# Optimization experiments

Hardware: AMD Instinct MI355X
Metric: run time of the kernel (lower is better)

The kernel has to match this reference:

```python
import jax, jax.numpy as jnp
import numpy as np

# IO parameters (aihwkit-style preset)
INP_BOUND = 1.0
INP_RES = 1.0 / 254.0      # 8-bit DAC: 2^8 - 2 levels
OUT_BOUND = 12.0
OUT_RES = 1.0 / 510.0      # 9-bit ADC: 2^9 - 2 levels
OUT_NOISE = 0.06
OUT_SCALE = 1.0
MAX_BM_FACTOR = 1000.0
MAX_BM_RES = 0.25
INP_RES_EFF = 2.0 * INP_BOUND * INP_RES  # effective input grid step (bm escape test)


def _quantize_st(x, res, bound):
    # UniformQuantize: round to grid of step (res * 2 * bound), straight-through grad
    r = (1.0 / res if res > 1.0 else res) * 2.0 * bound
    q = jnp.round(x / r) * r
    return x + jax.lax.stop_gradient(q - x)


def _one_pass(input_, weight, nm, reduction, rnd, key):
    """One analog MVM pass at a given bound-management reduction factor."""
    scale = 1.0 / (nm * reduction)                      # [m, 1]
    x = input_ * scale                                  # noise/bound managed input
    x = _quantize_st(x, INP_RES, INP_BOUND)             # DAC discretization
    x = jnp.clip(x, -INP_BOUND, INP_BOUND)              # DAC clipping
    out = x @ weight.T                                  # [m, out_size] analog GEMM
    noise = OUT_NOISE * jax.random.normal(
        jax.random.fold_in(key, rnd), out.shape, out.dtype)
    out = out + noise                                   # output (ADC) noise
    out = _quantize_st(out, OUT_RES, OUT_BOUND)         # ADC discretization
    not_clipping = jnp.all((out <= OUT_BOUND) & (out >= -OUT_BOUND))
    out = jnp.clip(out, -OUT_BOUND, OUT_BOUND)          # ADC saturation
    return not_clipping, out


def setup_inputs() -> dict:
    key = jax.random.key(0)
    k1, k2 = jax.random.split(key)
    input_ = jax.random.normal(k1, (8192, 4096), jnp.float32)
    # 0.1 std weights -> outputs mostly within ADC bound after 1-2 bm rounds
    weight = 0.1 * jax.random.normal(k2, (4096, 4096), jnp.float32)
    return {"input_": input_, "weight": weight}


def reference(input_, weight):
    key = jax.random.key(42)
    # noise management: ABS_MAX over the input dimension (nm_thres <= 0 -> no clamp)
    nm = jnp.max(jnp.abs(input_), axis=-1, keepdims=True)
    nm = jnp.where(nm <= 0.0, 1.0, nm)
    out_shape = input_.shape[:-1] + (weight.shape[0],)

    def cond(c):
        return ~c[2]

    def body(c):
        rnd, red, _, _ = c
        red = red * 2.0          # reduction_due_to_bound_management *= 2
        rnd = rnd + 1
        passed, out = _one_pass(input_, weight, nm, red, rnd, key)
        passed = passed | (red > MAX_BM_FACTOR) | (red > MAX_BM_RES / INP_RES_EFF)
        return (rnd, red, passed, out)

    init = (jnp.int32(0), jnp.float32(0.5), jnp.array(False),
            jnp.zeros(out_shape, input_.dtype))
    _, red, _, out = jax.lax.while_loop(cond, body, init)
    # undo the input scaling: output *= out_scale / scale = out_scale * nm * red
    return out * (OUT_SCALE * nm * red)
```

## Files before the change

### kernel.cpp

```cpp
#include <hip/hip_runtime.h>
#include <stdint.h>


#define MM 8192
#define KK 4096
#define NN 4096
#define TOTAL_OUT ((size_t)MM * (size_t)NN)
#define GEMM_BLOCKS 2048
#define NT (KK / 64)

typedef __attribute__((ext_vector_type(4))) float f32x4;
typedef __attribute__((ext_vector_type(8))) short bf16x8;
typedef __attribute__((ext_vector_type(8))) unsigned short u16x8;

#define R_IN_F ((float)(2.0 / 254.0))
#define R_OUT_F ((float)(24.0 / 510.0))

struct BmState {
  int done;
  float red_final;
  int viol[8];
  int ctr[8];
};

__host__ __device__ __forceinline__ uint32_t tf_rotl(uint32_t v, int r) {
  return (v << r) | (v >> (32 - r));
}

__host__ __device__ __forceinline__ void threefry2x32(uint32_t k0, uint32_t k1,
                                                      uint32_t x0, uint32_t x1,
                                                      uint32_t &o0, uint32_t &o1) {
  uint32_t ks2 = k0 ^ k1 ^ 0x1BD11BDAu;
  x0 += k0; x1 += k1;
#define TF_R(r) { x0 += x1; x1 = tf_rotl(x1, r); x1 ^= x0; }
  TF_R(13) TF_R(15) TF_R(26) TF_R(6)
  x0 += k1; x1 += ks2 + 1u;
  TF_R(17) TF_R(29) TF_R(16) TF_R(24)
  x0 += ks2; x1 += k0 + 2u;
  TF_R(13) TF_R(15) TF_R(26) TF_R(6)
  x0 += k0; x1 += k1 + 3u;
  TF_R(17) TF_R(29) TF_R(16) TF_R(24)
  x0 += k1; x1 += ks2 + 4u;
  TF_R(13) TF_R(15) TF_R(26) TF_R(6)
  x0 += ks2; x1 += k0 + 5u;
#undef TF_R
  o0 = x0; o1 = x1;
}

__device__ __forceinline__ float erfinv_xla(float x) {
  float w = -log1pf(-x * x);
  float p;
  if (w < 5.0f) {
    w = w - 2.5f;
    p = 2.81022636e-08f;
    p = fmaf(p, w, 3.43273939e-07f);
    p = fmaf(p, w, -3.5233877e-06f);
    p = fmaf(p, w, -4.39150654e-06f);
    p = fmaf(p, w, 0.00021858087f);
    p = fmaf(p, w, -0.00125372503f);
    p = fmaf(p, w, -0.00417768164f);
    p = fmaf(p, w, 0.246640727f);
    p = fmaf(p, w, 1.50140941f);
  } else {
    w = sqrtf(w) - 3.0f;
    p = -0.000200214257f;
    p = fmaf(p, w, 0.000100950558f);
    p = fmaf(p, w, 0.00134934322f);
    p = fmaf(p, w, -0.00367342844f);
    p = fmaf(p, w, 0.00573950773f);
    p = fmaf(p, w, -0.0076224613f);
    p = fmaf(p, w, 0.00943887047f);
    p = fmaf(p, w, 1.00167406f);
    p = fmaf(p, w, 2.83297682f);
  }
  return p * x;
}

__device__ __forceinline__ float noise_from_bits(uint32_t bits) {
  uint32_t fb = (bits >> 9) | 0x3f800000u;
  float f = __uint_as_float(fb) - 1.0f;
  const float lo = -0.99999994f;
  float u = f * 2.0f + lo;
  u = fmaxf(lo, u);
  return 0.06f * (1.41421356f * erfinv_xla(u));
}

__device__ __forceinline__ unsigned short bf16_rne(float f) {
  uint32_t x = __float_as_uint(f);
  x += 0x7fffu + ((x >> 16) & 1u);
  return (unsigned short)(x >> 16);
}

__device__ __forceinline__ float dac_quant(float v, float s) {
  float x = v * s;
  float t = x / R_IN_F;
  float k = rintf(t);
  return fminf(127.0f, fmaxf(-127.0f, k));
}

__device__ __forceinline__ u16x8 quant8(float4 a, float4 b, float s) {
  u16x8 o;
  o[0] = bf16_rne(dac_quant(a.x, s));
  o[1] = bf16_rne(dac_quant(a.y, s));
  o[2] = bf16_rne(dac_quant(a.z, s));
  o[3] = bf16_rne(dac_quant(a.w, s));
  o[4] = bf16_rne(dac_quant(b.x, s));
  o[5] = bf16_rne(dac_quant(b.y, s));
  o[6] = bf16_rne(dac_quant(b.z, s));
  o[7] = bf16_rne(dac_quant(b.w, s));
  return o;
}

__device__ __forceinline__ u16x8 conv8(float4 a, float4 b) {
  u16x8 o;
  o[0] = bf16_rne(a.x); o[1] = bf16_rne(a.y); o[2] = bf16_rne(a.z); o[3] = bf16_rne(a.w);
  o[4] = bf16_rne(b.x); o[5] = bf16_rne(b.y); o[6] = bf16_rne(b.z); o[7] = bf16_rne(b.w);
  return o;
}

__device__ __forceinline__ float adc_one(float gval, size_t idx, float sc,
                                         uint32_t fk0, uint32_t fk1, bool &bad) {
  uint32_t w0, w1;
  threefry2x32(fk0, fk1, 0u, (uint32_t)idx, w0, w1);
  float o = R_IN_F * gval + noise_from_bits(w0 ^ w1);
  float q = rintf(o / R_OUT_F) * R_OUT_F;
  float z = o + (q - o);
  bad = bad || (z > 12.0f) || (z < -12.0f);
  z = fminf(12.0f, fmaxf(-12.0f, z));
  return z * sc;
}

__device__ __forceinline__ void fin_tail(BmState *st, int pass, float red, int nblocks,
                                         bool bad) {
  unsigned long long vb = __ballot(bad ? 1 : 0);
  if (vb != 0ull && (threadIdx.x & 63) == 0) atomicOr(&st->viol[pass], 1);
  __syncthreads();
  if (threadIdx.x == 0) {
    __threadfence();
    int prev = atomicAdd(&st->ctr[pass], 1);
    if (prev == nblocks - 1) {
      int viol = atomicOr(&st->viol[pass], 0);
      bool ok = (viol == 0) || (red > 1000.0f) || (red > 31.75f);
      if (ok) {
        st->done = 1;
        st->red_final = red;
      }
    }
  }
}

__global__ __launch_bounds__(256) void k_rowquant(const float *__restrict__ in,
                                                  float *__restrict__ nm,
                                                  unsigned short *__restrict__ ab,
                                                  BmState *st) {
  if (blockIdx.x == 0 && threadIdx.x == 0) {
    st->done = 0;
    st->red_final = 0.0f;
    for (int i = 0; i < 8; ++i) { st->viol[i] = 0; st->ctr[i] = 0; }
  }
  const int row = blockIdx.x;
  const float *r = in + (size_t)row * KK;
  const int t = threadIdx.x;
  float4 a0 = *(const float4 *)(r + t * 8);
  float4 a1 = *(const float4 *)(r + t * 8 + 4);
  float4 b0 = *(const float4 *)(r + 2048 + t * 8);
  float4 b1 = *(const float4 *)(r + 2048 + t * 8 + 4);
  float m = 0.0f;
  m = fmaxf(m, fmaxf(fmaxf(fabsf(a0.x), fabsf(a0.y)), fmaxf(fabsf(a0.z), fabsf(a0.w))));
  m = fmaxf(m, fmaxf(fmaxf(fabsf(a1.x), fabsf(a1.y)), fmaxf(fabsf(a1.z), fabsf(a1.w))));
  m = fmaxf(m, fmaxf(fmaxf(fabsf(b0.x), fabsf(b0.y)), fmaxf(fabsf(b0.z), fabsf(b0.w))));
  m = fmaxf(m, fmaxf(fmaxf(fabsf(b1.x), fabsf(b1.y)), fmaxf(fabsf(b1.z), fabsf(b1.w))));
#pragma unroll
  for (int off = 32; off > 0; off >>= 1) m = fmaxf(m, __shfl_down(m, off));
  __shared__ float wm[4];
  if ((t & 63) == 0) wm[t >> 6] = m;
  __syncthreads();
  const float mm = fmaxf(fmaxf(wm[0], wm[1]), fmaxf(wm[2], wm[3]));
  const float nmv = (mm <= 0.0f) ? 1.0f : mm;
  if (t == 0) nm[row] = nmv;
  const float s = 1.0f / (nmv * 1.0f);
  unsigned short *o = ab + (size_t)row * KK;
  *(u16x8 *)(o + t * 8) = quant8(a0, a1, s);
  *(u16x8 *)(o + 2048 + t * 8) = quant8(b0, b1, s);
}

__global__ __launch_bounds__(256) void k_rowmax(const float *__restrict__ in,
                                                float *__restrict__ nm, BmState *st) {
  if (blockIdx.x == 0 && threadIdx.x == 0) {
    st->done = 0;
    st->red_final = 0.0f;
    for (int i = 0; i < 8; ++i) { st->viol[i] = 0; st->ctr[i] = 0; }
  }
  const int row = blockIdx.x;
  const float4 *r = (const float4 *)(in + (size_t)row * KK);
  const int t = threadIdx.x;
  float m = 0.0f;
#pragma unroll
  for (int i = 0; i < 4; ++i) {
    float4 v = r[t + i * 256];
    m = fmaxf(m, fmaxf(fmaxf(fabsf(v.x), fabsf(v.y)), fmaxf(fabsf(v.z), fabsf(v.w))));
  }
#pragma unroll
  for (int off = 32; off > 0; off >>= 1) m = fmaxf(m, __shfl_down(m, off));
  __shared__ float wm[4];
  if ((t & 63) == 0) wm[t >> 6] = m;
  __syncthreads();
  if (t == 0) {
    m = fmaxf(fmaxf(wm[0], wm[1]), fmaxf(wm[2], wm[3]));
    nm[row] = (m <= 0.0f) ? 1.0f : m;
  }
}

__global__ __launch_bounds__(256) void k_wconv(const float *__restrict__ w,
                                               unsigned short *__restrict__ wb) {
  const size_t idx = ((size_t)blockIdx.x * 256 + threadIdx.x) * 8;
  float4 a = *(const float4 *)(w + idx);
  float4 b = *(const float4 *)(w + idx + 4);
  *(u16x8 *)(wb + idx) = conv8(a, b);
}

__device__ __forceinline__ void async16(const void *g, void *l) {
  __builtin_amdgcn_global_load_lds((const __attribute__((address_space(1))) uint32_t *)g,
                                   (__attribute__((address_space(3))) uint32_t *)l,
                                   16, 0, 0);
}

__global__ __launch_bounds__(512, 1) void k_gemm(const unsigned short *__restrict__ A,
                                                 const unsigned short *__restrict__ B,
                                                 float *__restrict__ C) {
  __shared__ unsigned short As[2][256 * 64];
  __shared__ unsigned short Bs[2][256 * 64];
  const int tid = threadIdx.x;
  const int lane = tid & 63;
  const int wv = tid >> 6;
  const int wr = wv >> 2;
  const int wc = wv & 3;
  const int brow = blockIdx.y * 256;
  const int bcol = blockIdx.x * 256;

  f32x4 acc[8][4];
#pragma unroll
  for (int m = 0; m < 8; ++m)
#pragma unroll
    for (int n = 0; n < 4; ++n) acc[m][n] = (f32x4){0.f, 0.f, 0.f, 0.f};

  int sr[4], sk8[4];
#pragma unroll
  for (int i = 0; i < 4; ++i) {
    const int u = i * 512 + tid;
    sr[i] = u >> 3;
    sk8[i] = ((u & 7) ^ (sr[i] & 7)) * 8;
  }

#define STAGE(buf, kt)                                                                 \
  {                                                                                    \
    _Pragma("unroll") for (int i = 0; i < 4; ++i) {                                    \
      const int ub = i * 512 + wv * 64;                \
      async16(A + (size_t)(brow + sr[i]) * KK + (kt) * 64 + sk8[i],                    \
              (char *)As[buf] + (size_t)ub * 16);                                      \
      async16(B + (size_t)(bcol + sr[i]) * KK + (kt) * 64 + sk8[i],                    \
              (char *)Bs[buf] + (size_t)ub * 16);                                      \
    }                                                                                  \
  }

  STAGE(0, 0);

  const int r16 = lane & 15;
  const int kg = (lane >> 4) * 8;

#pragma unroll 2
  for (int kt = 0; kt < NT; ++kt) {
    const int cur = kt & 1;
    if (kt + 1 < NT) {
      STAGE(cur ^ 1, kt + 1);
      asm volatile("s_waitcnt vmcnt(8)" ::: "memory");
    } else {
      asm volatile("s_waitcnt vmcnt(0)" ::: "memory");
    }
    __builtin_amdgcn_s_barrier();

#pragma unroll
    for (int kk = 0; kk < 64; kk += 32) {
      const int ck = (kk + kg) >> 3;
      bf16x8 af[8], bg[4];
#pragma unroll
      for (int m = 0; m < 8; ++m) {
        const int ra = wr * 128 + m * 16 + r16;
        af[m] = *(const bf16x8 *)(As[cur] + ra * 64 + ((ck ^ (ra & 7)) << 3));
      }
#pragma unroll
      for (int n = 0; n < 4; ++n) {
        const int rb = wc * 64 + n * 16 + r16;
        bg[n] = *(const bf16x8 *)(Bs[cur] + rb * 64 + ((ck ^ (rb & 7)) << 3));
      }
#pragma unroll
      for (int m = 0; m < 8; ++m)
#pragma unroll
        for (int n = 0; n < 4; ++n)
          acc[m][n] = __builtin_amdgcn_mfma_f32_16x16x32_bf16(af[m], bg[n], acc[m][n], 0, 0, 0);
    }
    __builtin_amdgcn_sched_barrier(0);
    __builtin_amdgcn_s_barrier();
  }
#undef STAGE

  const int c16 = lane & 15;
  const int q4 = (lane >> 4) * 4;
#pragma unroll
  for (int m = 0; m < 8; ++m) {
    const int row = brow + wr * 128 + m * 16 + q4;
#pragma unroll
    for (int n = 0; n < 4; ++n) {
      const int col = bcol + wc * 64 + n * 16 + c16;
      float *cp = C + (size_t)row * NN + col;
      cp[0 * (size_t)NN] = acc[m][n][0];
      cp[1 * (size_t)NN] = acc[m][n][1];
      cp[2 * (size_t)NN] = acc[m][n][2];
      cp[3 * (size_t)NN] = acc[m][n][3];
    }
  }
}

__global__ __launch_bounds__(256) void k_epi(float *__restrict__ out,
                                             const float *__restrict__ nm,
                                             BmState *__restrict__ st, int pass, float red,
                                             uint32_t fk0, uint32_t fk1) {
  const size_t idx = ((size_t)blockIdx.x * 256 + threadIdx.x) * 8;
  const int row = (int)(idx >> 12);
  const float sc = nm[row] * red;
  float4 a = *(const float4 *)(out + idx);
  float4 b = *(const float4 *)(out + idx + 4);
  float v[8] = {a.x, a.y, a.z, a.w, b.x, b.y, b.z, b.w};
  bool bad = false;
#pragma unroll
  for (int j = 0; j < 8; ++j) v[j] = adc_one(v[j], idx + j, sc, fk0, fk1, bad);
  *(float4 *)(out + idx) = make_float4(v[0], v[1], v[2], v[3]);
  *(float4 *)(out + idx + 4) = make_float4(v[4], v[5], v[6], v[7]);
  unsigned long long vb = __ballot(bad ? 1 : 0);
  if (vb != 0ull && (threadIdx.x & 63) == 0) atomicOr(&st->viol[pass], 1);
}

__global__ void k_fin(BmState *st, int pass, float red) {
  if (st->done) return;
  bool ok = (st->viol[pass] == 0) || (red > 1000.0f) || (red > 31.75f);
  if (ok) {
    st->done = 1;
    st->red_final = red;
  }
}

__global__ __launch_bounds__(256) void k_retry(const float *__restrict__ Af,
                                               const float *__restrict__ Bf,
                                               const float *__restrict__ nm, float red,
                                               float *__restrict__ C,
                                               BmState *__restrict__ st, int pass,
                                               uint32_t fk0, uint32_t fk1) {
  if (st->done) return;
  __shared__ unsigned short As[128 * 64];
  __shared__ unsigned short Bs[128 * 64];
  const int tid = threadIdx.x;
  const int lane = tid & 63;
  const int wv = tid >> 6;
  const int wr = wv >> 1, wc = wv & 1;
  const int brow = blockIdx.y * 128;
  const int bcol = blockIdx.x * 128;

  f32x4 acc[4][4];
#pragma unroll
  for (int m = 0; m < 4; ++m)
#pragma unroll
    for (int n = 0; n < 4; ++n) acc[m][n] = (f32x4){0.f, 0.f, 0.f, 0.f};

  float sA[4];
#pragma unroll
  for (int i = 0; i < 4; ++i) {
    int u = i * 256 + tid;
    sA[i] = 1.0f / (nm[brow + (u >> 3)] * red);
  }

  for (int kt = 0; kt < KK; kt += 64) {
#pragma unroll
    for (int i = 0; i < 4; ++i) {
      const int u = i * 256 + tid;
      const int r = u >> 3, k8 = (u & 7) * 8;
      {
        const float *g = Af + (size_t)(brow + r) * KK + kt + k8;
        float4 x = *(const float4 *)g, y = *(const float4 *)(g + 4);
        *(u16x8 *)(As + r * 64 + k8) = quant8(x, y, sA[i]);
      }
      {
        const float *g = Bf + (size_t)(bcol + r) * KK + kt + k8;
        float4 x = *(const float4 *)g, y = *(const float4 *)(g + 4);
        *(u16x8 *)(Bs + r * 64 + k8) = conv8(x, y);
      }
    }
    __syncthreads();

    const int r16 = lane & 15;
    const int kg = (lane >> 4) * 8;
#pragma unroll
    for (int kk = 0; kk < 64; kk += 32) {
      bf16x8 af[4], bg[4];
#pragma unroll
      for (int m = 0; m < 4; ++m)
        af[m] = *(const bf16x8 *)(As + (wr * 64 + m * 16 + r16) * 64 + kk + kg);
#pragma unroll
      for (int n = 0; n < 4; ++n)
        bg[n] = *(const bf16x8 *)(Bs + (wc * 64 + n * 16 + r16) * 64 + kk + kg);
#pragma unroll
      for (int m = 0; m < 4; ++m)
#pragma unroll
        for (int n = 0; n < 4; ++n)
          acc[m][n] = __builtin_amdgcn_mfma_f32_16x16x32_bf16(af[m], bg[n], acc[m][n], 0, 0, 0);
    }
    __syncthreads();
  }

  const int c16 = lane & 15;
  const int q4 = (lane >> 4) * 4;
  bool bad = false;
#pragma unroll
  for (int m = 0; m < 4; ++m) {
    const int row0 = brow + wr * 64 + m * 16 + q4;
#pragma unroll
    for (int j = 0; j < 4; ++j) {
      const int row = row0 + j;
      const float sc = nm[row] * red;
#pragma unroll
      for (int n = 0; n < 4; ++n) {
        const int col = bcol + wc * 64 + n * 16 + c16;
        const size_t idx = (size_t)row * NN + col;
        C[idx] = adc_one(acc[m][n][j], idx, sc, fk0, fk1, bad);
      }
    }
  }
  fin_tail(st, pass, red, GEMM_BLOCKS, bad);
}

extern "C" void kernel_launch(void *const *d_in, const int *in_sizes, int n_in,
                              void *d_out, int out_size, void *d_ws, size_t ws_size,
                              hipStream_t stream) {
  const float *input = (const float *)d_in[0];
  const float *weight = (const float *)d_in[1];
  if (n_in >= 2 && in_sizes[0] < in_sizes[1]) {
    const float *t = input; input = weight; weight = t;
  }
  float *out = (float *)d_out;
  char *ws = (char *)d_ws;
  BmState *st = (BmState *)ws;
  float *nm = (float *)(ws + 4096);
  unsigned short *Ab = (unsigned short *)(ws + 36864);
  unsigned short *Wb = Ab + (size_t)MM * KK;
  const size_t need = 36864 + ((size_t)MM * KK + (size_t)NN * KK) * 2;
  const bool fast = ws_size >= need;

  uint32_t fk[8][2];
  for (int p = 1; p <= 6; ++p) threefry2x32(0u, 42u, 0u, (uint32_t)p, fk[p][0], fk[p][1]);

  if (fast) {
    k_rowquant<<<dim3(MM), dim3(256), 0, stream>>>(input, nm, Ab, st);
    k_wconv<<<dim3((NN * (size_t)KK) / 2048), dim3(256), 0, stream>>>(weight, Wb);
    k_gemm<<<dim3(NN / 256, MM / 256), dim3(512), 0, stream>>>(Ab, Wb, out);
    k_epi<<<dim3((int)(TOTAL_OUT / 2048)), dim3(256), 0, stream>>>(out, nm, st, 1, 1.0f,
                                                                   fk[1][0], fk[1][1]);
    k_fin<<<dim3(1), dim3(1), 0, stream>>>(st, 1, 1.0f);
  } else {
    k_rowmax<<<dim3(MM), dim3(256), 0, stream>>>(input, nm, st);
    k_retry<<<dim3(NN / 128, MM / 128), dim3(256), 0, stream>>>(
        input, weight, nm, 1.0f, out, st, 1, fk[1][0], fk[1][1]);
  }

  float red = 2.0f;
  for (int p = 2; p <= 6; ++p, red *= 2.0f) {
    k_retry<<<dim3(NN / 128, MM / 128), dim3(256), 0, stream>>>(
        input, weight, nm, red, out, st, p, fk[p][0], fk[p][1]);
  }
}
```

Before: 495.9 us.

## Fuse ADC epilogue into GEMM and merge input/weight prep kernels

The separate ADC epilogue kernel (noise, quantize, clip, violation detection) now runs inside the GEMM's register epilogue, so the 128 MB fp32 output is no longer written, re-read and rewritten. The row-quantize and weight-convert kernels are merged into one launch to save a launch and let the two workloads overlap. In exchange the GEMM epilogue carries the per-element RNG work, which raises register pressure and lengthens the tail of the GEMM.

```diff
diff --git a/kernel.cpp b/kernel.cpp
--- a/kernel.cpp
+++ b/kernel.cpp
@@ -149,39 +149,48 @@
   }
 }
 
-__global__ __launch_bounds__(256) void k_rowquant(const float *__restrict__ in,
-                                                  float *__restrict__ nm,
-                                                  unsigned short *__restrict__ ab,
-                                                  BmState *st) {
-  if (blockIdx.x == 0 && threadIdx.x == 0) {
-    st->done = 0;
-    st->red_final = 0.0f;
-    for (int i = 0; i < 8; ++i) { st->viol[i] = 0; st->ctr[i] = 0; }
-  }
-  const int row = blockIdx.x;
-  const float *r = in + (size_t)row * KK;
+__global__ __launch_bounds__(256) void k_prep(const float *__restrict__ in,
+                                              const float *__restrict__ w,
+                                              float *__restrict__ nm,
+                                              unsigned short *__restrict__ ab,
+                                              unsigned short *__restrict__ wb,
+                                              BmState *st) {
   const int t = threadIdx.x;
-  float4 a0 = *(const float4 *)(r + t * 8);
-  float4 a1 = *(const float4 *)(r + t * 8 + 4);
-  float4 b0 = *(const float4 *)(r + 2048 + t * 8);
-  float4 b1 = *(const float4 *)(r + 2048 + t * 8 + 4);
-  float m = 0.0f;
-  m = fmaxf(m, fmaxf(fmaxf(fabsf(a0.x), fabsf(a0.y)), fmaxf(fabsf(a0.z), fabsf(a0.w))));
-  m = fmaxf(m, fmaxf(fmaxf(fabsf(a1.x), fabsf(a1.y)), fmaxf(fabsf(a1.z), fabsf(a1.w))));
-  m = fmaxf(m, fmaxf(fmaxf(fabsf(b0.x), fabsf(b0.y)), fmaxf(fabsf(b0.z), fabsf(b0.w))));
-  m = fmaxf(m, fmaxf(fmaxf(fabsf(b1.x), fabsf(b1.y)), fmaxf(fabsf(b1.z), fabsf(b1.w))));
-#pragma unroll
-  for (int off = 32; off > 0; off >>= 1) m = fmaxf(m, __shfl_down(m, off));
-  __shared__ float wm[4];
-  if ((t & 63) == 0) wm[t >> 6] = m;
-  __syncthreads();
-  const float mm = fmaxf(fmaxf(wm[0], wm[1]), fmaxf(wm[2], wm[3]));
-  const float nmv = (mm <= 0.0f) ? 1.0f : mm;
-  if (t == 0) nm[row] = nmv;
-  const float s = 1.0f / (nmv * 1.0f);
-  unsigned short *o = ab + (size_t)row * KK;
-  *(u16x8 *)(o + t * 8) = quant8(a0, a1, s);
-  *(u16x8 *)(o + 2048 + t * 8) = quant8(b0, b1, s);
+  if (blockIdx.x < MM) {
+    if (blockIdx.x == 0 && t == 0) {
+      st->done = 0;
+      st->red_final = 0.0f;
+      for (int i = 0; i < 8; ++i) { st->viol[i] = 0; st->ctr[i] = 0; }
+    }
+    const int row = blockIdx.x;
+    const float *r = in + (size_t)row * KK;
+    float4 a0 = *(const float4 *)(r + t * 8);
+    float4 a1 = *(const float4 *)(r + t * 8 + 4);
+    float4 b0 = *(const float4 *)(r + 2048 + t * 8);
+    float4 b1 = *(const float4 *)(r + 2048 + t * 8 + 4);
+    float m = 0.0f;
+    m = fmaxf(m, fmaxf(fmaxf(fabsf(a0.x), fabsf(a0.y)), fmaxf(fabsf(a0.z), fabsf(a0.w))));
+    m = fmaxf(m, fmaxf(fmaxf(fabsf(a1.x), fabsf(a1.y)), fmaxf(fabsf(a1.z), fabsf(a1.w))));
+    m = fmaxf(m, fmaxf(fmaxf(fabsf(b0.x), fabsf(b0.y)), fmaxf(fabsf(b0.z), fabsf(b0.w))));
+    m = fmaxf(m, fmaxf(fmaxf(fabsf(b1.x), fabsf(b1.y)), fmaxf(fabsf(b1.z), fabsf(b1.w))));
+#pragma unroll
+    for (int off = 32; off > 0; off >>= 1) m = fmaxf(m, __shfl_down(m, off));
+    __shared__ float wm[4];
+    if ((t & 63) == 0) wm[t >> 6] = m;
+    __syncthreads();
+    const float mm = fmaxf(fmaxf(wm[0], wm[1]), fmaxf(wm[2], wm[3]));
+    const float nmv = (mm <= 0.0f) ? 1.0f : mm;
+    if (t == 0) nm[row] = nmv;
+    const float s = 1.0f / (nmv * 1.0f);
+    unsigned short *o = ab + (size_t)row * KK;
+    *(u16x8 *)(o + t * 8) = quant8(a0, a1, s);
+    *(u16x8 *)(o + 2048 + t * 8) = quant8(b0, b1, s);
+  } else {
+    const size_t idx = ((size_t)(blockIdx.x - MM) * 256 + t) * 8;
+    float4 a = *(const float4 *)(w + idx);
+    float4 b = *(const float4 *)(w + idx + 4);
+    *(u16x8 *)(wb + idx) = conv8(a, b);
+  }
 }
 
 __global__ __launch_bounds__(256) void k_rowmax(const float *__restrict__ in,
@@ -211,14 +220,6 @@
   }
 }
 
-__global__ __launch_bounds__(256) void k_wconv(const float *__restrict__ w,
-                                               unsigned short *__restrict__ wb) {
-  const size_t idx = ((size_t)blockIdx.x * 256 + threadIdx.x) * 8;
-  float4 a = *(const float4 *)(w + idx);
-  float4 b = *(const float4 *)(w + idx + 4);
-  *(u16x8 *)(wb + idx) = conv8(a, b);
-}
-
 __device__ __forceinline__ void async16(const void *g, void *l) {
   __builtin_amdgcn_global_load_lds((const __attribute__((address_space(1))) uint32_t *)g,
                                    (__attribute__((address_space(3))) uint32_t *)l,
@@ -227,7 +228,10 @@
 
 __global__ __launch_bounds__(512, 1) void k_gemm(const unsigned short *__restrict__ A,
                                                  const unsigned short *__restrict__ B,
-                                                 float *__restrict__ C) {
+                                                 const float *__restrict__ nm,
+                                                 float *__restrict__ C,
+                                                 BmState *__restrict__ st, int pass,
+                                                 float red, uint32_t fk0, uint32_t fk1) {
   __shared__ unsigned short As[2][256 * 64];
   __shared__ unsigned short Bs[2][256 * 64];
   const int tid = threadIdx.x;
@@ -306,38 +310,24 @@
 
   const int c16 = lane & 15;
   const int q4 = (lane >> 4) * 4;
+  bool bad = false;
 #pragma unroll
   for (int m = 0; m < 8; ++m) {
-    const int row = brow + wr * 128 + m * 16 + q4;
-#pragma unroll
-    for (int n = 0; n < 4; ++n) {
-      const int col = bcol + wc * 64 + n * 16 + c16;
-      float *cp = C + (size_t)row * NN + col;
-      cp[0 * (size_t)NN] = acc[m][n][0];
-      cp[1 * (size_t)NN] = acc[m][n][1];
-      cp[2 * (size_t)NN] = acc[m][n][2];
-      cp[3 * (size_t)NN] = acc[m][n][3];
-    }
-  }
-}
-
-__global__ __launch_bounds__(256) void k_epi(float *__restrict__ out,
-                                             const float *__restrict__ nm,
-                                             BmState *__restrict__ st, int pass, float red,
-                                             uint32_t fk0, uint32_t fk1) {
-  const size_t idx = ((size_t)blockIdx.x * 256 + threadIdx.x) * 8;
-  const int row = (int)(idx >> 12);
-  const float sc = nm[row] * red;
-  float4 a = *(const float4 *)(out + idx);
-  float4 b = *(const float4 *)(out + idx + 4);
-  float v[8] = {a.x, a.y, a.z, a.w, b.x, b.y, b.z, b.w};
-  bool bad = false;
-#pragma unroll
-  for (int j = 0; j < 8; ++j) v[j] = adc_one(v[j], idx + j, sc, fk0, fk1, bad);
-  *(float4 *)(out + idx) = make_float4(v[0], v[1], v[2], v[3]);
-  *(float4 *)(out + idx + 4) = make_float4(v[4], v[5], v[6], v[7]);
+    const int row0 = brow + wr * 128 + m * 16 + q4;
+#pragma unroll
+    for (int j = 0; j < 4; ++j) {
+      const int row = row0 + j;
+      const float sc = nm[row] * red;
+#pragma unroll
+      for (int n = 0; n < 4; ++n) {
+        const int col = bcol + wc * 64 + n * 16 + c16;
+        const size_t idx = (size_t)row * NN + col;
+        C[idx] = adc_one(acc[m][n][j], idx, sc, fk0, fk1, bad);
+      }
+    }
+  }
   unsigned long long vb = __ballot(bad ? 1 : 0);
-  if (vb != 0ull && (threadIdx.x & 63) == 0) atomicOr(&st->viol[pass], 1);
+  if (vb != 0ull && lane == 0) atomicOr(&st->viol[pass], 1);
 }
 
 __global__ void k_fin(BmState *st, int pass, float red) {
@@ -458,11 +448,10 @@
   for (int p = 1; p <= 6; ++p) threefry2x32(0u, 42u, 0u, (uint32_t)p, fk[p][0], fk[p][1]);
 
   if (fast) {
-    k_rowquant<<<dim3(MM), dim3(256), 0, stream>>>(input, nm, Ab, st);
-    k_wconv<<<dim3((NN * (size_t)KK) / 2048), dim3(256), 0, stream>>>(weight, Wb);
-    k_gemm<<<dim3(NN / 256, MM / 256), dim3(512), 0, stream>>>(Ab, Wb, out);
-    k_epi<<<dim3((int)(TOTAL_OUT / 2048)), dim3(256), 0, stream>>>(out, nm, st, 1, 1.0f,
-                                                                   fk[1][0], fk[1][1]);
+    k_prep<<<dim3(MM + (NN * (size_t)KK) / 2048), dim3(256), 0, stream>>>(
+        input, weight, nm, Ab, Wb, st);
+    k_gemm<<<dim3(NN / 256, MM / 256), dim3(512), 0, stream>>>(
+        Ab, Wb, nm, out, st, 1, 1.0f, fk[1][0], fk[1][1]);
     k_fin<<<dim3(1), dim3(1), 0, stream>>>(st, 1, 1.0f);
   } else {
     k_rowmax<<<dim3(MM), dim3(256), 0, stream>>>(input, nm, st);
```

Result: slower. 608.5 us (+22.7%).
